# Kernel optimization log

Hardware: AMD Instinct MI355X
Metric: run time of the kernel (lower is better)

## Reference

```python
import jax, jax.numpy as jnp
import numpy as np

K, D, N, W, OUT = 16, 2, 16384, 256, 1
TW = 0.2  # fixed_transition_width


def setup_inputs() -> dict:
    key = jax.random.key(0)
    ks = jax.random.split(key, 9)
    # 4x4 grid of subdomains over [0,1]^2
    edges = np.linspace(0.0, 1.0, 5).astype(np.float32)
    mins = np.array([[edges[i], edges[j]] for i in range(4) for j in range(4)], np.float32)
    maxs = mins + 0.25

    def init_w(k, shape, fan_in):
        return jax.random.normal(k, shape, jnp.float32) / np.sqrt(fan_in).astype(np.float32)

    return {
        "x": jax.random.uniform(ks[0], (N, D), jnp.float32),
        "W0": init_w(ks[1], (K, D, W), D),
        "b0": jnp.zeros((K, W), jnp.float32),
        "W1": init_w(ks[2], (K, W, W), W),
        "b1": jnp.zeros((K, W), jnp.float32),
        "W2": init_w(ks[3], (K, W, W), W),
        "b2": jnp.zeros((K, W), jnp.float32),
        "W3": init_w(ks[4], (K, W, OUT), W),
        "b3": jnp.zeros((K, OUT), jnp.float32),
        "xmins": jnp.asarray(mins),
        "xmaxs": jnp.asarray(maxs),
    }


def _cosine_window(xmins, xmaxs, wmin, x):
    """Normalized cosine partition-of-unity weights. x:[N,D], xmins/xmaxs:[K,D] -> [N,K]."""
    # smooth ramp 0->1 over [xmin-w, xmin+w] and 1->0 over [xmax-w, xmax+w], per dim
    t_l = jnp.clip((x[None] - (xmins - wmin)[:, None]) / (2.0 * wmin), 0.0, 1.0)  # [K,N,D]
    t_r = jnp.clip(((xmaxs + wmin)[:, None] - x[None]) / (2.0 * wmin), 0.0, 1.0)
    w_raw = jnp.prod(0.25 * (1.0 - jnp.cos(jnp.pi * t_l)) * (1.0 - jnp.cos(jnp.pi * t_r)), axis=-1)  # [K,N]
    w = w_raw / (jnp.sum(w_raw, axis=0, keepdims=True) + 1e-9)
    return w.T  # [N,K]


def reference(x, W0, b0, W1, b1, W2, b2, W3, b3, xmins, xmaxs):
    all_w = _cosine_window(xmins, xmaxs, TW, x)  # [N,K]
    # per-subdomain normalization of x to [-1,1]
    center = (xmins + xmaxs) * 0.5
    scale = jnp.maximum((xmaxs - xmins) * 0.5, 1e-9)
    xn = (x[None] - center[:, None]) / scale[:, None]  # [K,N,D]
    # batched small MLPs (one per subdomain), tanh hidden activations
    h = jnp.tanh(jnp.einsum('knd,kdw->knw', xn, W0) + b0[:, None])
    h = jnp.tanh(jnp.einsum('knw,kwv->knv', h, W1) + b1[:, None])
    h = jnp.tanh(jnp.einsum('knw,kwv->knv', h, W2) + b2[:, None])
    sub = jnp.einsum('knw,kwo->kno', h, W3) + b3[:, None]  # [K,N,OUT]
    # window-weighted combine; ansatz is identity in the NN output
    return jnp.einsum('nk,kno->no', all_w, sub)  # [N,OUT]
```

## Files before the change

### kernel.cpp

```cpp
#include <hip/hip_runtime.h>
#include <stdint.h>

#define TWF 0.2f
#define NPTS 16384

typedef __attribute__((ext_vector_type(8))) short short8;
typedef __attribute__((ext_vector_type(4))) float floatx4;

__device__ __forceinline__ short f2bf(float f){
  unsigned u = __float_as_uint(f);
  u += 0x7fff + ((u >> 16) & 1);
  return (short)(u >> 16);
}
__device__ __forceinline__ float bf2f(short s){
  return __uint_as_float(((unsigned)(unsigned short)s) << 16);
}
__device__ __forceinline__ float fast_tanh(float x){
  float e = __builtin_amdgcn_exp2f(x * 2.885390082f);
  float r = __builtin_amdgcn_rcpf(e + 1.f);
  return fmaf(-2.f, r, 1.f);
}
__device__ __forceinline__ float cospi_t(float t){
  return __builtin_amdgcn_cosf(t * 0.5f);
}
__device__ __forceinline__ int swz(int m, int j){
  return m * 256 + ((((j >> 3) ^ (m & 7)) << 3) | (j & 7));
}

#define WS_W      0
#define WS_CNT    (4u<<20)
#define WS_ILIST  ((4u<<20) + 4096u)
#define WS_WLIST  ((5u<<20) + 4096u)
#define CNT(k)    counts[(k) * 32]

__global__ __launch_bounds__(256) void prep_fused(
    const float* __restrict__ W1, const float* __restrict__ W2,
    const float* __restrict__ x,  const float* __restrict__ xmins,
    const float* __restrict__ xmaxs, short* __restrict__ dst,
    int* __restrict__ counts, int* __restrict__ ilist, float* __restrict__ wlist,
    float* __restrict__ out){
  if (blockIdx.x < 1024){
    int gid = blockIdx.x * 256 + threadIdx.x;
    int lane = gid & 63; int rest = gid >> 6;
    int jt = rest & 15; rest >>= 4;
    int ks = rest & 7;  rest >>= 3;
    int k  = rest & 15; int mat = rest >> 4;
    const float* W = mat ? W2 : W1;
    int j   = jt * 16 + (lane & 15);
    int kk0 = ks * 32 + (lane >> 4) * 8;
    short8 v;
    #pragma unroll
    for (int jj = 0; jj < 8; jj++)
      v[jj] = f2bf(W[k * 65536 + (kk0 + jj) * 256 + j]);
    *(short8*)(dst + (size_t)gid * 8) = v;
  } else {
    __shared__ int s_wcnt[4];
    __shared__ int s_base;
    int gid  = (blockIdx.x - 1024) * 256 + threadIdx.x;
    int t    = threadIdx.x;
    int lane = t & 63, wave = t >> 6;
    out[gid] = 0.f;
    float px = x[gid * 2 + 0], py = x[gid * 2 + 1];
    float wr[16]; float sum = 0.f;
    #pragma unroll
    for (int k = 0; k < 16; k++){
      float w = 1.f;
      #pragma unroll
      for (int d = 0; d < 2; d++){
        float xv = d ? py : px;
        float mn = xmins[k * 2 + d], mx = xmaxs[k * 2 + d];
        float tl = fminf(fmaxf((xv - (mn - TWF)) * (1.f / (2.f * TWF)), 0.f), 1.f);
        float tr = fminf(fmaxf(((mx + TWF) - xv) * (1.f / (2.f * TWF)), 0.f), 1.f);
        w *= 0.25f * (1.f - cospi_t(tl)) * (1.f - cospi_t(tr));
      }
      wr[k] = w; sum += w;
    }
    float inv = 1.f / (sum + 1e-9f);
    #pragma unroll 1
    for (int kk = 0; kk < 16; kk++){
      int k = (kk + blockIdx.x) & 15;
      bool act = wr[k] > 0.f;
      unsigned long long mask = __ballot(act);
      if (lane == 0) s_wcnt[wave] = (int)__popcll(mask);
      __syncthreads();
      int tot = s_wcnt[0] + s_wcnt[1] + s_wcnt[2] + s_wcnt[3];
      int wpre = 0;
      #pragma unroll
      for (int w = 0; w < 4; w++) wpre += (w < wave) ? s_wcnt[w] : 0;
      if (t == 0) s_base = atomicAdd(&CNT(k), tot);
      __syncthreads();
      if (act){
        int pos = s_base + wpre + (int)__popcll(mask & ((1ull << lane) - 1ull));
        ilist[k * NPTS + pos] = gid;
        wlist[k * NPTS + pos] = wr[k] * inv;
      }
    }
  }
}

__global__ __launch_bounds__(256, 3) void fbpinn_main(
    const float* __restrict__ x,  const float* __restrict__ W0, const float* __restrict__ b0,
    const float* __restrict__ b1, const float* __restrict__ b2,
    const float* __restrict__ W3, const float* __restrict__ b3,
    const float* __restrict__ xmins, const float* __restrict__ xmaxs,
    const short* __restrict__ wsw, const int* __restrict__ counts,
    const int* __restrict__ ilist, const float* __restrict__ wlist,
    float* __restrict__ out)
{
  __shared__ short lds_h[64 * 256];
  __shared__ float s_xn[64 * 2];
  __shared__ float s_win[64];
  __shared__ int   s_pidx[64];
  __shared__ float s_w3[256];
  __shared__ float s_w0[512];

  const int t    = threadIdx.x;
  const int lane = t & 63;
  const int wave = t >> 6;
  const int col  = lane & 15;
  const int quad = lane >> 4;

  int tb[17]; tb[0] = 0;
  #pragma unroll
  for (int kk = 0; kk < 16; kk++) tb[kk + 1] = tb[kk] + ((CNT(kk) + 63) >> 6);
  const int total = tb[16];

  for (int tile = blockIdx.x; tile < total; tile += gridDim.x){
    int k = 0;
    #pragma unroll
    for (int kk = 1; kk < 16; kk++) k += (tile >= tb[kk]);
    const int base = (tile - tb[k]) * 64;
    const int cnt  = CNT(k);

    __syncthreads();

    s_w3[t] = W3[k * 256 + t];
    s_w0[t] = W0[k * 512 + t];
    s_w0[256 + t] = W0[k * 512 + 256 + t];
    if (t < 64){
      int gi = base + t;
      bool valid = gi < cnt;
      int pidx = valid ? ilist[k * NPTS + gi] : 0;
      float w  = valid ? wlist[k * NPTS + gi] : 0.f;
      s_pidx[t] = pidx;
      s_win[t]  = w;
      float px = x[pidx * 2 + 0], py = x[pidx * 2 + 1];
      float cx = (xmins[k * 2 + 0] + xmaxs[k * 2 + 0]) * 0.5f;
      float cy = (xmins[k * 2 + 1] + xmaxs[k * 2 + 1]) * 0.5f;
      float sx = fmaxf((xmaxs[k * 2 + 0] - xmins[k * 2 + 0]) * 0.5f, 1e-9f);
      float sy = fmaxf((xmaxs[k * 2 + 1] - xmins[k * 2 + 1]) * 0.5f, 1e-9f);
      s_xn[t * 2 + 0] = (px - cx) / sx;
      s_xn[t * 2 + 1] = (py - cy) / sy;
    }
    __syncthreads();

    {
      short8 bfr[4], afr[4];
      #pragma unroll
      for (int jtl = 0; jtl < 4; jtl++){
        int j = (wave * 4 + jtl) * 16 + col;
        short8 b;
        #pragma unroll
        for (int i = 0; i < 8; i++) b[i] = 0;
        b[0] = (quad == 0) ? f2bf(s_w0[j])       : (short)0;
        b[1] = (quad == 0) ? f2bf(s_w0[256 + j]) : (short)0;
        bfr[jtl] = b;
      }
      #pragma unroll
      for (int mt = 0; mt < 4; mt++){
        int m = mt * 16 + col;
        short8 a;
        #pragma unroll
        for (int i = 0; i < 8; i++) a[i] = 0;
        a[0] = (quad == 0) ? f2bf(s_xn[m * 2 + 0]) : (short)0;
        a[1] = (quad == 0) ? f2bf(s_xn[m * 2 + 1]) : (short)0;
        afr[mt] = a;
      }
      floatx4 acc[4][4];
      #pragma unroll
      for (int a = 0; a < 4; a++)
        #pragma unroll
        for (int b = 0; b < 4; b++)
          acc[a][b] = (floatx4){0.f, 0.f, 0.f, 0.f};
      #pragma unroll
      for (int mt = 0; mt < 4; mt++)
        #pragma unroll
        for (int jtl = 0; jtl < 4; jtl++)
          acc[mt][jtl] = __builtin_amdgcn_mfma_f32_16x16x32_bf16(afr[mt], bfr[jtl], acc[mt][jtl], 0, 0, 0);
      #pragma unroll
      for (int jtl = 0; jtl < 4; jtl++){
        int j = (wave * 4 + jtl) * 16 + col;
        float bb = b0[k * 256 + j];
        #pragma unroll
        for (int mt = 0; mt < 4; mt++){
          #pragma unroll
          for (int r = 0; r < 4; r++){
            int m = mt * 16 + quad * 4 + r;
            lds_h[swz(m, j)] = f2bf(fast_tanh(acc[mt][jtl][r] + bb));
          }
        }
      }
      __syncthreads();
    }

    #pragma unroll 1
    for (int layer = 0; layer < 2; layer++){
      const short8* wb = (const short8*)(wsw + (size_t)layer * 1048576)
                         + ((size_t)(k * 8) * 16 + wave * 4) * 64 + lane;
      const float*  bp = layer ? b2 : b1;
      floatx4 acc[4][4];
      #pragma unroll
      for (int a = 0; a < 4; a++)
        #pragma unroll
        for (int b = 0; b < 4; b++)
          acc[a][b] = (floatx4){0.f, 0.f, 0.f, 0.f};

      short8 bcur[4];
      #pragma unroll
      for (int jtl = 0; jtl < 4; jtl++) bcur[jtl] = wb[jtl * 64];

      #pragma unroll
      for (int ks = 0; ks < 8; ks++){
        short8 bnxt[4];
        if (ks < 7){
          #pragma unroll
          for (int jtl = 0; jtl < 4; jtl++)
            bnxt[jtl] = wb[(ks + 1) * 1024 + jtl * 64];
        }
        short8 afr[4];
        #pragma unroll
        for (int mt = 0; mt < 4; mt++){
          int m   = mt * 16 + col;
          int pos = (ks * 4 + quad) ^ (m & 7);
          afr[mt] = *(const short8*)&lds_h[m * 256 + pos * 8];
        }
        #pragma unroll
        for (int mt = 0; mt < 4; mt++)
          #pragma unroll
          for (int jtl = 0; jtl < 4; jtl++)
            acc[mt][jtl] = __builtin_amdgcn_mfma_f32_16x16x32_bf16(afr[mt], bcur[jtl], acc[mt][jtl], 0, 0, 0);
        if (ks < 7){
          #pragma unroll
          for (int jtl = 0; jtl < 4; jtl++) bcur[jtl] = bnxt[jtl];
        }
      }
      __syncthreads();

      #pragma unroll
      for (int jtl = 0; jtl < 4; jtl++){
        int j = (wave * 4 + jtl) * 16 + col;
        float bb = bp[k * 256 + j];
        #pragma unroll
        for (int mt = 0; mt < 4; mt++){
          #pragma unroll
          for (int r = 0; r < 4; r++){
            int m = mt * 16 + quad * 4 + r;
            lds_h[swz(m, j)] = f2bf(fast_tanh(acc[mt][jtl][r] + bb));
          }
        }
      }
      __syncthreads();
    }

    {
      int m = t >> 2, q = t & 3;
      float dot = 0.f;
      #pragma unroll
      for (int cc = 0; cc < 8; cc++){
        int ci  = q * 8 + cc;
        int pos = ci ^ (m & 7);
        short8 hv = *(const short8*)&lds_h[m * 256 + pos * 8];
        #pragma unroll
        for (int jj = 0; jj < 8; jj++)
          dot = fmaf(bf2f(hv[jj]), s_w3[ci * 8 + jj], dot);
      }
      dot += __shfl_xor(dot, 1);
      dot += __shfl_xor(dot, 2);
      if (q == 0 && s_win[m] != 0.f)
        atomicAdd(&out[s_pidx[m]], s_win[m] * (dot + b3[k]));
    }
  }
}

extern "C" void kernel_launch(void* const* d_in, const int* in_sizes, int n_in,
                              void* d_out, int out_size, void* d_ws, size_t ws_size,
                              hipStream_t stream){
  const float* x     = (const float*)d_in[0];
  const float* W0    = (const float*)d_in[1];
  const float* b0    = (const float*)d_in[2];
  const float* W1    = (const float*)d_in[3];
  const float* b1    = (const float*)d_in[4];
  const float* W2    = (const float*)d_in[5];
  const float* b2    = (const float*)d_in[6];
  const float* W3    = (const float*)d_in[7];
  const float* b3    = (const float*)d_in[8];
  const float* xmins = (const float*)d_in[9];
  const float* xmaxs = (const float*)d_in[10];
  float* out = (float*)d_out;

  char* ws = (char*)d_ws;
  short* wsw   = (short*)(ws + WS_W);
  int*   cnts  = (int*)  (ws + WS_CNT);
  int*   ilist = (int*)  (ws + WS_ILIST);
  float* wlist = (float*)(ws + WS_WLIST);

  (void)hipMemsetAsync(cnts, 0, 4096, stream);
  prep_fused<<<1024 + NPTS / 256, 256, 0, stream>>>(W1, W2, x, xmins, xmaxs,
                                                    wsw, cnts, ilist, wlist, out);
  fbpinn_main<<<640, 256, 0, stream>>>(x, W0, b0, b1, b2, W3, b3, xmins, xmaxs,
                                       wsw, cnts, ilist, wlist, out);
}
```

Before: 153.6 us.

## Transpose MFMA operands so hidden stores pack into vectorized bf16 writes

Swaps the MFMA operand roles so weights become the A operand and activations the B operand. Each lane's four accumulator values then fall on consecutive hidden features of one point and can be converted with v_cvt_pk_bf16 and written as a single 8-byte LDS store, replacing sixteen scalar 2-byte stores. Biases are loaded as float4 once per layer. The change also raises the launch-bounds occupancy hint from 3 to 4 and the grid from 640 to 2048 blocks, which adds register pressure and more blocks that may exit with no work.

Result: faster. 147.6 us (-3.9%).

```diff
diff --git a/kernel.cpp b/kernel.cpp
--- a/kernel.cpp
+++ b/kernel.cpp
@@ -23,8 +23,10 @@
 __device__ __forceinline__ float cospi_t(float t){
   return __builtin_amdgcn_cosf(t * 0.5f);
 }
-__device__ __forceinline__ int swz(int m, int j){
-  return m * 256 + ((((j >> 3) ^ (m & 7)) << 3) | (j & 7));
+__device__ __forceinline__ unsigned cvt_pk_bf16(float lo, float hi){
+  unsigned r;
+  asm("v_cvt_pk_bf16_f32 %0, %1, %2" : "=v"(r) : "v"(lo), "v"(hi));
+  return r;
 }
 
 #define WS_W      0
@@ -98,7 +100,28 @@
   }
 }
 
-__global__ __launch_bounds__(256, 3) void fbpinn_main(
+__device__ __forceinline__ void store_h_packed(
+    short* lds_h, const floatx4 (&acc)[4][4], const floatx4 (&bb)[4],
+    int wave, int quad, int col){
+  #pragma unroll
+  for (int rt = 0; rt < 4; rt++){
+    const int j0    = (wave * 4 + rt) * 16 + quad * 4;
+    const int cbase = j0 >> 3;
+    const int off   = j0 & 7;
+    #pragma unroll
+    for (int ct = 0; ct < 4; ct++){
+      const int m = ct * 16 + col;
+      float t0 = fast_tanh(acc[rt][ct][0] + bb[rt][0]);
+      float t1 = fast_tanh(acc[rt][ct][1] + bb[rt][1]);
+      float t2 = fast_tanh(acc[rt][ct][2] + bb[rt][2]);
+      float t3 = fast_tanh(acc[rt][ct][3] + bb[rt][3]);
+      uint2 v = make_uint2(cvt_pk_bf16(t0, t1), cvt_pk_bf16(t2, t3));
+      *(uint2*)&lds_h[m * 256 + ((cbase ^ (m & 7)) << 3) + off] = v;
+    }
+  }
+}
+
+__global__ __launch_bounds__(256, 4) void fbpinn_main(
     const float* __restrict__ x,  const float* __restrict__ W0, const float* __restrict__ b0,
     const float* __restrict__ b1, const float* __restrict__ b2,
     const float* __restrict__ W3, const float* __restrict__ b3,
@@ -155,27 +178,31 @@
     __syncthreads();
 
     {
-      short8 bfr[4], afr[4];
-      #pragma unroll
-      for (int jtl = 0; jtl < 4; jtl++){
-        int j = (wave * 4 + jtl) * 16 + col;
+      short8 wfr[4], xfr[4];
+      #pragma unroll
+      for (int rt = 0; rt < 4; rt++){
+        int j = (wave * 4 + rt) * 16 + col;
+        short8 a;
+        #pragma unroll
+        for (int i = 0; i < 8; i++) a[i] = 0;
+        a[0] = (quad == 0) ? f2bf(s_w0[j])       : (short)0;
+        a[1] = (quad == 0) ? f2bf(s_w0[256 + j]) : (short)0;
+        wfr[rt] = a;
+      }
+      #pragma unroll
+      for (int ct = 0; ct < 4; ct++){
+        int m = ct * 16 + col;
         short8 b;
         #pragma unroll
         for (int i = 0; i < 8; i++) b[i] = 0;
-        b[0] = (quad == 0) ? f2bf(s_w0[j])       : (short)0;
-        b[1] = (quad == 0) ? f2bf(s_w0[256 + j]) : (short)0;
-        bfr[jtl] = b;
-      }
-      #pragma unroll
-      for (int mt = 0; mt < 4; mt++){
-        int m = mt * 16 + col;
-        short8 a;
-        #pragma unroll
-        for (int i = 0; i < 8; i++) a[i] = 0;
-        a[0] = (quad == 0) ? f2bf(s_xn[m * 2 + 0]) : (short)0;
-        a[1] = (quad == 0) ? f2bf(s_xn[m * 2 + 1]) : (short)0;
-        afr[mt] = a;
-      }
+        b[0] = (quad == 0) ? f2bf(s_xn[m * 2 + 0]) : (short)0;
+        b[1] = (quad == 0) ? f2bf(s_xn[m * 2 + 1]) : (short)0;
+        xfr[ct] = b;
+      }
+      floatx4 bb[4];
+      #pragma unroll
+      for (int rt = 0; rt < 4; rt++)
+        bb[rt] = *(const floatx4*)&b0[k * 256 + (wave * 4 + rt) * 16 + quad * 4];
       floatx4 acc[4][4];
       #pragma unroll
       for (int a = 0; a < 4; a++)
@@ -183,23 +210,11 @@
         for (int b = 0; b < 4; b++)
           acc[a][b] = (floatx4){0.f, 0.f, 0.f, 0.f};
       #pragma unroll
-      for (int mt = 0; mt < 4; mt++)
-        #pragma unroll
-        for (int jtl = 0; jtl < 4; jtl++)
-          acc[mt][jtl] = __builtin_amdgcn_mfma_f32_16x16x32_bf16(afr[mt], bfr[jtl], acc[mt][jtl], 0, 0, 0);
-      #pragma unroll
-      for (int jtl = 0; jtl < 4; jtl++){
-        int j = (wave * 4 + jtl) * 16 + col;
-        float bb = b0[k * 256 + j];
-        #pragma unroll
-        for (int mt = 0; mt < 4; mt++){
-          #pragma unroll
-          for (int r = 0; r < 4; r++){
-            int m = mt * 16 + quad * 4 + r;
-            lds_h[swz(m, j)] = f2bf(fast_tanh(acc[mt][jtl][r] + bb));
-          }
-        }
-      }
+      for (int rt = 0; rt < 4; rt++)
+        #pragma unroll
+        for (int ct = 0; ct < 4; ct++)
+          acc[rt][ct] = __builtin_amdgcn_mfma_f32_16x16x32_bf16(wfr[rt], xfr[ct], acc[rt][ct], 0, 0, 0);
+      store_h_packed(lds_h, acc, bb, wave, quad, col);
       __syncthreads();
     }
 
@@ -208,6 +223,10 @@
       const short8* wb = (const short8*)(wsw + (size_t)layer * 1048576)
                          + ((size_t)(k * 8) * 16 + wave * 4) * 64 + lane;
       const float*  bp = layer ? b2 : b1;
+      floatx4 bb[4];
+      #pragma unroll
+      for (int rt = 0; rt < 4; rt++)
+        bb[rt] = *(const floatx4*)&bp[k * 256 + (wave * 4 + rt) * 16 + quad * 4];
       floatx4 acc[4][4];
       #pragma unroll
       for (int a = 0; a < 4; a++)
@@ -215,50 +234,38 @@
         for (int b = 0; b < 4; b++)
           acc[a][b] = (floatx4){0.f, 0.f, 0.f, 0.f};
 
-      short8 bcur[4];
-      #pragma unroll
-      for (int jtl = 0; jtl < 4; jtl++) bcur[jtl] = wb[jtl * 64];
+      short8 wcur[4];
+      #pragma unroll
+      for (int rt = 0; rt < 4; rt++) wcur[rt] = wb[rt * 64];
 
       #pragma unroll
       for (int ks = 0; ks < 8; ks++){
-        short8 bnxt[4];
+        short8 wnxt[4];
         if (ks < 7){
           #pragma unroll
-          for (int jtl = 0; jtl < 4; jtl++)
-            bnxt[jtl] = wb[(ks + 1) * 1024 + jtl * 64];
+          for (int rt = 0; rt < 4; rt++)
+            wnxt[rt] = wb[(ks + 1) * 1024 + rt * 64];
         }
-        short8 afr[4];
-        #pragma unroll
-        for (int mt = 0; mt < 4; mt++){
-          int m   = mt * 16 + col;
+        short8 hfr[4];
+        #pragma unroll
+        for (int ct = 0; ct < 4; ct++){
+          int m   = ct * 16 + col;
           int pos = (ks * 4 + quad) ^ (m & 7);
-          afr[mt] = *(const short8*)&lds_h[m * 256 + pos * 8];
+          hfr[ct] = *(const short8*)&lds_h[m * 256 + pos * 8];
         }
         #pragma unroll
-        for (int mt = 0; mt < 4; mt++)
+        for (int rt = 0; rt < 4; rt++)
           #pragma unroll
-          for (int jtl = 0; jtl < 4; jtl++)
-            acc[mt][jtl] = __builtin_amdgcn_mfma_f32_16x16x32_bf16(afr[mt], bcur[jtl], acc[mt][jtl], 0, 0, 0);
+          for (int ct = 0; ct < 4; ct++)
+            acc[rt][ct] = __builtin_amdgcn_mfma_f32_16x16x32_bf16(wcur[rt], hfr[ct], acc[rt][ct], 0, 0, 0);
         if (ks < 7){
           #pragma unroll
-          for (int jtl = 0; jtl < 4; jtl++) bcur[jtl] = bnxt[jtl];
+          for (int rt = 0; rt < 4; rt++) wcur[rt] = wnxt[rt];
         }
       }
       __syncthreads();
 
-      #pragma unroll
-      for (int jtl = 0; jtl < 4; jtl++){
-        int j = (wave * 4 + jtl) * 16 + col;
-        float bb = bp[k * 256 + j];
-        #pragma unroll
-        for (int mt = 0; mt < 4; mt++){
-          #pragma unroll
-          for (int r = 0; r < 4; r++){
-            int m = mt * 16 + quad * 4 + r;
-            lds_h[swz(m, j)] = f2bf(fast_tanh(acc[mt][jtl][r] + bb));
-          }
-        }
-      }
+      store_h_packed(lds_h, acc, bb, wave, quad, col);
       __syncthreads();
     }
 
@@ -307,6 +314,6 @@
   (void)hipMemsetAsync(cnts, 0, 4096, stream);
   prep_fused<<<1024 + NPTS / 256, 256, 0, stream>>>(W1, W2, x, xmins, xmaxs,
                                                     wsw, cnts, ilist, wlist, out);
-  fbpinn_main<<<640, 256, 0, stream>>>(x, W0, b0, b1, b2, W3, b3, xmins, xmaxs,
-                                       wsw, cnts, ilist, wlist, out);
-}
+  fbpinn_main<<<2048, 256, 0, stream>>>(x, W0, b0, b1, b2, W3, b3, xmins, xmaxs,
+                                        wsw, cnts, ilist, wlist, out);
+}
```
